# Kernel optimization log

Hardware: AMD Instinct MI355X
Metric: run time of the kernel (lower is better)

The kernel has to match this reference:

```python
import jax, jax.numpy as jnp
import numpy as np

TGT, BSZ, E = 2048, 4, 1024
NUM_HEADS = 16
HEAD_DIM = E // NUM_HEADS


def setup_inputs() -> dict:
    key = jax.random.key(0)
    ks = jax.random.split(key, 5)
    return {
        "query": jax.random.normal(ks[0], (TGT, BSZ, E), dtype=jnp.float32),
        "key": jax.random.normal(ks[1], (TGT, BSZ, E), dtype=jnp.float32),
        "value": jax.random.normal(ks[2], (TGT, BSZ, E), dtype=jnp.float32),
        "in_proj_weight": jax.random.normal(ks[3], (3 * E, E), dtype=jnp.float32) * (1.0 / np.sqrt(E)),
        "in_proj_bias": jnp.zeros((3 * E,), dtype=jnp.float32),
        "out_proj_weight": jax.random.normal(ks[4], (E, E), dtype=jnp.float32) * (1.0 / np.sqrt(E)),
        "out_proj_bias": jnp.zeros((E,), dtype=jnp.float32),
    }


def reference(query, key, value, in_proj_weight, in_proj_bias, out_proj_weight, out_proj_bias):
    tgt_len, bsz, embed_dim = query.shape
    src_len = key.shape[0]
    h, hd = NUM_HEADS, embed_dim // NUM_HEADS

    w_q, w_k, w_v = jnp.split(in_proj_weight, 3, axis=0)
    b_q, b_k, b_v = jnp.split(in_proj_bias, 3, axis=0)
    q = query @ w_q.T + b_q   # (Nt, B, E)
    k = key @ w_k.T + b_k     # (Ns, B, E)
    v = value @ w_v.T + b_v

    # (L, B, E) -> (B*H, L, hd)
    q = q.reshape(tgt_len, bsz * h, hd).transpose(1, 0, 2)
    k = k.reshape(src_len, bsz * h, hd).transpose(1, 0, 2)
    v = v.reshape(src_len, bsz * h, hd).transpose(1, 0, 2)

    q = q / jnp.sqrt(jnp.asarray(hd, dtype=q.dtype))
    attn = jnp.einsum('bte,bse->bts', q, k)          # (B*H, Nt, Ns)
    attn = jax.nn.softmax(attn, axis=-1)
    out = jnp.einsum('bts,bse->bte', attn, v)        # (B*H, Nt, hd)

    out = out.transpose(1, 0, 2).reshape(tgt_len, bsz, embed_dim)
    out = out @ out_proj_weight.T + out_proj_bias    # (Nt, B, out_dim)

    avg_weights = attn.reshape(bsz, h, tgt_len, src_len).mean(axis=1)
    return (out, avg_weights)
```

## Files before the change

kernel.cpp:

```cpp
#include <hip/hip_runtime.h>
#include <hip/hip_bf16.h>
#include <hip/hip_fp16.h>

#define TGT 2048
#define BSZ 4
#define EMB 1024
#define NH  16
#define HD  64
#define NTOK (TGT*BSZ)
#define BH   (BSZ*NH)

typedef unsigned short u16;
typedef __attribute__((ext_vector_type(8)))  short        s16x8;
typedef __attribute__((ext_vector_type(8)))  _Float16     f16x8;
typedef __attribute__((ext_vector_type(2)))  _Float16     f16x2;
typedef __attribute__((ext_vector_type(2)))  __fp16       fp16x2;
typedef __attribute__((ext_vector_type(4)))  float        f32x4;
typedef __attribute__((ext_vector_type(16))) float        f32x16;
typedef __attribute__((ext_vector_type(4)))  unsigned int u32x4;

#define MFMA_BF16(a,b,c)  __builtin_amdgcn_mfma_f32_16x16x32_bf16(a,b,c,0,0,0)
#define MFMA_F16(a,b,c)   __builtin_amdgcn_mfma_f32_16x16x32_f16(a,b,c,0,0,0)
#define MFMA32_F16(a,b,c) __builtin_amdgcn_mfma_f32_32x32x16_f16(a,b,c,0,0,0)

#define GLOAD_LDS16(gsrc, ldst) \
  __builtin_amdgcn_global_load_lds((const __attribute__((address_space(1))) unsigned int*)(gsrc), \
                                   (__attribute__((address_space(3))) unsigned int*)(ldst), 16, 0, 0)

__device__ __forceinline__ void split_one(float x, u16& h, u16& l) {
  __hip_bfloat16 hb = __float2bfloat16(x);
  float hf = __bfloat162float(hb);
  __hip_bfloat16 lb = __float2bfloat16(x - hf);
  h = *reinterpret_cast<u16*>(&hb);
  l = *reinterpret_cast<u16*>(&lb);
}

__global__ __launch_bounds__(256) void split_kernel(const float* __restrict__ x,
    u16* __restrict__ hi, u16* __restrict__ lo, int n4) {
  int i = blockIdx.x * 256 + threadIdx.x;
  if (i >= n4) return;
  float4 v = reinterpret_cast<const float4*>(x)[i];
  ushort4 h, l;
  split_one(v.x, h.x, l.x);
  split_one(v.y, h.y, l.y);
  split_one(v.z, h.z, l.z);
  split_one(v.w, h.w, l.w);
  reinterpret_cast<ushort4*>(hi)[i] = h;
  reinterpret_cast<ushort4*>(lo)[i] = l;
}

template<int EPI>
__global__ __launch_bounds__(256) void gemm_split(
    const u16* __restrict__ Ah, const u16* __restrict__ Al,
    const u16* __restrict__ Bh, const u16* __restrict__ Bl,
    const float* __restrict__ bias, float scale, void* __restrict__ outp, int K)
{
  __shared__ __align__(16) u16 As[128*64];
  __shared__ __align__(16) u16 Bs[128*64];
  const int tid  = threadIdx.x;
  const int bm0  = blockIdx.y * 128;
  const int bn0  = blockIdx.x * 128;
  const int wave = tid >> 6, lane = tid & 63, lr = lane & 15, lg = lane >> 4;

  f32x4 zero = {0.f, 0.f, 0.f, 0.f};
  f32x4 acc[2][8];
  #pragma unroll
  for (int i = 0; i < 2; i++)
    #pragma unroll
    for (int j = 0; j < 8; j++) acc[i][j] = zero;

  const u16* srcA[4];
  const u16* srcB[4];
  #pragma unroll
  for (int j = 0; j < 4; j++) {
    int gi  = tid + j*256;
    int row = gi >> 3;
    int lgc = (gi & 7) ^ (row & 7);
    const u16* baA = (lgc < 4) ? Ah : Al;
    const u16* baB = (lgc < 4) ? Bh : Bl;
    srcA[j] = baA + (size_t)(bm0 + row)*K + (lgc & 3)*8;
    srcB[j] = baB + (size_t)(bn0 + row)*K + (lgc & 3)*8;
  }
  char* AsB = (char*)As;
  char* BsB = (char*)Bs;
  const int ldsb = wave*1024;

  for (int kt = 0; kt < K; kt += 32) {
    __syncthreads();
    #pragma unroll
    for (int j = 0; j < 4; j++) {
      GLOAD_LDS16(srcA[j] + kt, AsB + ldsb + j*4096);
      GLOAD_LDS16(srcB[j] + kt, BsB + ldsb + j*4096);
    }
    __syncthreads();

    s16x8 ah[2], al2[2];
    #pragma unroll
    for (int mf = 0; mf < 2; mf++) {
      int row = wave*32 + mf*16 + lr;
      const char* rb = AsB + row*128;
      ah[mf]  = *(const s16x8*)(rb + (((lg    ) ^ (row & 7)) << 4));
      al2[mf] = *(const s16x8*)(rb + (((lg | 4) ^ (row & 7)) << 4));
    }
    #pragma unroll
    for (int nf = 0; nf < 8; nf++) {
      int row = nf*16 + lr;
      const char* rb = BsB + row*128;
      s16x8 bh8 = *(const s16x8*)(rb + (((lg    ) ^ (row & 7)) << 4));
      s16x8 bl8 = *(const s16x8*)(rb + (((lg | 4) ^ (row & 7)) << 4));
      #pragma unroll
      for (int mf = 0; mf < 2; mf++) {
        acc[mf][nf] = MFMA_BF16(al2[mf], bh8, acc[mf][nf]);
        acc[mf][nf] = MFMA_BF16(ah[mf],  bl8, acc[mf][nf]);
        acc[mf][nf] = MFMA_BF16(ah[mf],  bh8, acc[mf][nf]);
      }
    }
  }
  #pragma unroll
  for (int mf = 0; mf < 2; mf++)
    #pragma unroll
    for (int nf = 0; nf < 8; nf++)
      #pragma unroll
      for (int r = 0; r < 4; r++) {
        int m = bm0 + wave*32 + mf*16 + lg*4 + r;
        int n = bn0 + nf*16 + lr;
        float v = (acc[mf][nf][r] + bias[n]) * scale;
        if constexpr (EPI == 0) {
          int t = m >> 2, b = m & 3, h = n >> 6, d = n & 63;
          ((_Float16*)outp)[(size_t)((b*NH + h)*TGT + t)*HD + d] = (_Float16)v;
        } else if constexpr (EPI == 1) {
          int s = m >> 2, b = m & 3, h = n >> 6, d = n & 63;
          ((_Float16*)outp)[(size_t)((b*NH + h)*HD + d)*TGT + s] = (_Float16)v;
        } else {
          ((float*)outp)[(size_t)m*EMB + n] = v;
        }
      }
}

__global__ __launch_bounds__(256) void flash_kernel(
    const _Float16* __restrict__ Qf, const _Float16* __restrict__ Kf,
    const _Float16* __restrict__ Vt, u16* __restrict__ Oh, u16* __restrict__ Ol,
    float* __restrict__ lse)
{
  __shared__ __align__(16) _Float16 Ks[64*64];
  __shared__ __align__(16) _Float16 Vs[64*64];
  const int tid = threadIdx.x, wq = tid >> 6, lane = tid & 63;
  const int lt = lane & 31, hl = lane >> 5;
  const int bh = blockIdx.y, t0 = blockIdx.x * 128;
  const int b = bh >> 4, h = bh & 15;
  const int t = t0 + wq*32 + lt;

  f16x8 qf[4];
  #pragma unroll
  for (int kk = 0; kk < 4; kk++)
    qf[kk] = *(const f16x8*)&Qf[((size_t)bh*TGT + t)*HD + kk*16 + hl*8];

  float m_run = -1e30f, l_run = 0.f;
  f32x16 accO[2];
  #pragma unroll
  for (int i = 0; i < 16; i++) { accO[0][i] = 0.f; accO[1][i] = 0.f; }

  char* KsB = (char*)Ks;
  char* VsB = (char*)Vs;

  for (int s0 = 0; s0 < TGT; s0 += 64) {
    __syncthreads();
    #pragma unroll
    for (int j = 0; j < 2; j++) {
      int gi = tid + j*256;
      int row = gi >> 3, sg = (gi & 7) ^ (row & 7);
      GLOAD_LDS16(Kf + ((size_t)bh*TGT + s0 + row)*HD + sg*8, KsB + wq*1024 + j*4096);
      GLOAD_LDS16(Vt + ((size_t)bh*HD + row)*TGT + s0 + sg*8, VsB + wq*1024 + j*4096);
    }
    __syncthreads();

    f32x16 sacc[2];
    #pragma unroll
    for (int i = 0; i < 16; i++) { sacc[0][i] = 0.f; sacc[1][i] = 0.f; }
    #pragma unroll
    for (int sf = 0; sf < 2; sf++)
      #pragma unroll
      for (int kk = 0; kk < 4; kk++) {
        int row = sf*32 + lt;
        int g = (2*kk + hl) ^ (row & 7);
        f16x8 kfr = *(const f16x8*)(KsB + row*128 + g*16);
        sacc[sf] = MFMA32_F16(kfr, qf[kk], sacc[sf]);
      }

    float pm = -1e30f;
    #pragma unroll
    for (int sf = 0; sf < 2; sf++)
      #pragma unroll
      for (int r = 0; r < 16; r++) pm = fmaxf(pm, sacc[sf][r]);
    pm = fmaxf(pm, __shfl_xor(pm, 32, 64));
    float m_new = fmaxf(m_run, pm);
    float fsc = exp2f(m_run - m_new);
    float psum = 0.f;
    #pragma unroll
    for (int sf = 0; sf < 2; sf++)
      #pragma unroll
      for (int r = 0; r < 16; r++) {
        float p = exp2f(sacc[sf][r] - m_new);
        sacc[sf][r] = p;
        psum += p;
      }
    psum += __shfl_xor(psum, 32, 64);
    l_run = l_run * fsc + psum;
    m_run = m_new;
    accO[0] *= fsc;
    accO[1] *= fsc;

    #pragma unroll
    for (int sf = 0; sf < 2; sf++) {
      unsigned int P0[4], P1[4];
      #pragma unroll
      for (int q = 0; q < 4; q++) {
        union { fp16x2 h2; unsigned int u; } c0, c1;
        c0.h2 = __builtin_amdgcn_cvt_pkrtz(sacc[sf][4*q],     sacc[sf][4*q + 1]);
        c1.h2 = __builtin_amdgcn_cvt_pkrtz(sacc[sf][4*q + 2], sacc[sf][4*q + 3]);
        P0[q] = c0.u;
        P1[q] = c1.u;
      }
      #pragma unroll
      for (int mp = 0; mp < 2; mp++) {
        unsigned int a0 = P0[2*mp], b0 = P0[2*mp + 1];
        unsigned int a1 = P1[2*mp], b1 = P1[2*mp + 1];
        asm("v_permlane32_swap_b32 %0, %1" : "+v"(a0), "+v"(b0));
        asm("v_permlane32_swap_b32 %0, %1" : "+v"(a1), "+v"(b1));
        union { u32x4 u; f16x8 f; } pw;
        pw.u = (u32x4){a0, a1, b0, b1};
        const int m = sf*2 + mp;
        #pragma unroll
        for (int df = 0; df < 2; df++) {
          int row = df*32 + lt;
          int g = (2*m + hl) ^ (row & 7);
          f16x8 vfr = *(const f16x8*)(VsB + row*128 + g*16);
          accO[df] = MFMA32_F16(vfr, pw.f, accO[df]);
        }
      }
    }
  }

  float linv = 1.f / l_run;
  #pragma unroll
  for (int df = 0; df < 2; df++)
    #pragma unroll
    for (int q = 0; q < 4; q++) {
      ushort4 hs, ls;
      float o0 = accO[df][4*q]     * linv;
      float o1 = accO[df][4*q + 1] * linv;
      float o2 = accO[df][4*q + 2] * linv;
      float o3 = accO[df][4*q + 3] * linv;
      split_one(o0, hs.x, ls.x);
      split_one(o1, hs.y, ls.y);
      split_one(o2, hs.z, ls.z);
      split_one(o3, hs.w, ls.w);
      int d0 = 32*df + 8*q + 4*hl;
      size_t idx = ((size_t)t*BSZ + b)*EMB + h*HD + d0;
      *(ushort4*)&Oh[idx] = hs;
      *(ushort4*)&Ol[idx] = ls;
    }
  if (hl == 0)
    lse[(size_t)bh*TGT + t] = m_run + log2f(l_run);
}

__global__ __launch_bounds__(256) void avg_kernel(
    const _Float16* __restrict__ Qf, const _Float16* __restrict__ Kf,
    const float* __restrict__ lse, float* __restrict__ avgO)
{
  __shared__ __align__(16) _Float16 Qs[128][64];
  __shared__ __align__(16) _Float16 Ks[128][64];
  __shared__ float lses[NH][128];
  const int tid = threadIdx.x, wave = tid >> 6, lane = tid & 63, lr = lane & 15, lg = lane >> 4;

  int fid = blockIdx.x;
  int nid = (fid & 7) * 128 + (fid >> 3);
  int st = nid & 15, tt = (nid >> 4) & 15, b = nid >> 8;
  int s0 = st * 128, t0 = tt * 128;

  #pragma unroll
  for (int i = 0; i < 8; i++) {
    int idx = tid + i * 256;
    int hh = idx >> 7, t = idx & 127;
    lses[hh][t] = lse[(size_t)(b*NH + hh)*TGT + t0 + t];
  }

  f32x4 zero = {0.f, 0.f, 0.f, 0.f};
  f32x4 acc[2][8];
  #pragma unroll
  for (int i = 0; i < 2; i++)
    #pragma unroll
    for (int j = 0; j < 8; j++) acc[i][j] = zero;

  const int rQ = wave * 32;
  const int srcsub = (((lane & 7) ^ (lane >> 3)) << 4) + (lane >> 3) * 128;

  for (int h = 0; h < NH; h++) {
    __syncthreads();
    {
      const char* qb = (const char*)(Qf + ((size_t)(b*NH + h)*TGT + t0) * HD);
      const char* kb = (const char*)(Kf + ((size_t)(b*NH + h)*TGT + s0) * HD);
      const char* gb = (wave < 2) ? qb : kb;
      char* lb = (char*)((wave < 2) ? &Qs[0][0] : &Ks[0][0]);
      const int half = (wave & 1) * 8;
      #pragma unroll
      for (int j = 0; j < 8; j++) {
        int J = half + j;
        GLOAD_LDS16(gb + (size_t)J * 1024 + srcsub, lb + J * 1024);
      }
    }
    __syncthreads();

    float lsr[2][4];
    #pragma unroll
    for (int mf = 0; mf < 2; mf++)
      #pragma unroll
      for (int r = 0; r < 4; r++)
        lsr[mf][r] = lses[h][rQ + mf*16 + lg*4 + r];

    f16x8 aq[2][2];
    #pragma unroll
    for (int mf = 0; mf < 2; mf++)
      #pragma unroll
      for (int kf = 0; kf < 2; kf++) {
        int row = rQ + mf*16 + lr;
        int cb = ((kf*4 + lg) ^ (row & 7)) << 4;
        aq[mf][kf] = *(const f16x8*)((const char*)&Qs[0][0] + row*128 + cb);
      }
    #pragma unroll
    for (int nf = 0; nf < 8; nf++) {
      f32x4 s4[2] = {zero, zero};
      #pragma unroll
      for (int kf = 0; kf < 2; kf++) {
        int row = nf*16 + lr;
        int cb = ((kf*4 + lg) ^ (row & 7)) << 4;
        f16x8 bk = *(const f16x8*)((const char*)&Ks[0][0] + row*128 + cb);
        s4[0] = MFMA_F16(aq[0][kf], bk, s4[0]);
        s4[1] = MFMA_F16(aq[1][kf], bk, s4[1]);
      }
      #pragma unroll
      for (int mf = 0; mf < 2; mf++)
        #pragma unroll
        for (int r = 0; r < 4; r++)
          acc[mf][nf][r] += exp2f(s4[mf][r] - lsr[mf][r]);
    }
  }

  #pragma unroll
  for (int mf = 0; mf < 2; mf++)
    #pragma unroll
    for (int nf = 0; nf < 8; nf++)
      #pragma unroll
      for (int r = 0; r < 4; r++) {
        int ti = t0 + rQ + mf*16 + lg*4 + r;
        int sj = s0 + nf*16 + lr;
        avgO[((size_t)b*TGT + ti)*TGT + sj] = acc[mf][nf][r] * (1.f/16.f);
      }
}

extern "C" void kernel_launch(void* const* d_in, const int* in_sizes, int n_in,
                              void* d_out, int out_size, void* d_ws, size_t ws_size,
                              hipStream_t stream) {
  const float* query = (const float*)d_in[0];
  const float* key_  = (const float*)d_in[1];
  const float* value = (const float*)d_in[2];
  const float* ipw   = (const float*)d_in[3];
  const float* ipb   = (const float*)d_in[4];
  const float* opw   = (const float*)d_in[5];
  const float* opb   = (const float*)d_in[6];
  float* out = (float*)d_out;
  float* avg = out + (size_t)TGT*BSZ*EMB;

  char* ws = (char*)d_ws;
  size_t o = 0;
  auto alloc = [&](size_t bytes) { char* p = ws + o; o += bytes; return p; };
  u16* Wh  = (u16*)alloc((size_t)3*EMB*EMB*2);
  u16* Wl  = (u16*)alloc((size_t)3*EMB*EMB*2);
  u16* Woh = (u16*)alloc((size_t)EMB*EMB*2);
  u16* Wol = (u16*)alloc((size_t)EMB*EMB*2);
  u16* Xh  = (u16*)alloc((size_t)NTOK*EMB*2);
  u16* Xl  = (u16*)alloc((size_t)NTOK*EMB*2);
  _Float16* Qf = (_Float16*)alloc((size_t)NTOK*EMB*2);
  _Float16* Kf = (_Float16*)alloc((size_t)NTOK*EMB*2);
  _Float16* Vt = (_Float16*)alloc((size_t)NTOK*EMB*2);
  u16* OhA = (u16*)alloc((size_t)NTOK*EMB*2);
  u16* OlA = (u16*)alloc((size_t)NTOK*EMB*2);
  float* lseA = (float*)alloc((size_t)BH*TGT*4);
  (void)ws_size; (void)in_sizes; (void)n_in; (void)out_size;

  const float QSCALE = 0.18033688011112042f;

  split_kernel<<<3*EMB*EMB/1024, 256, 0, stream>>>(ipw, Wh, Wl, 3*EMB*EMB/4);
  split_kernel<<<EMB*EMB/1024, 256, 0, stream>>>(opw, Woh, Wol, EMB*EMB/4);

  dim3 ggrid(EMB/128, NTOK/128);
  split_kernel<<<NTOK*EMB/1024, 256, 0, stream>>>(query, Xh, Xl, NTOK*EMB/4);
  gemm_split<0><<<ggrid, 256, 0, stream>>>(Xh, Xl, Wh, Wl, ipb, QSCALE, (void*)Qf, EMB);
  split_kernel<<<NTOK*EMB/1024, 256, 0, stream>>>(key_, Xh, Xl, NTOK*EMB/4);
  gemm_split<0><<<ggrid, 256, 0, stream>>>(Xh, Xl, Wh + (size_t)EMB*EMB, Wl + (size_t)EMB*EMB,
                                           ipb + EMB, 1.0f, (void*)Kf, EMB);
  split_kernel<<<NTOK*EMB/1024, 256, 0, stream>>>(value, Xh, Xl, NTOK*EMB/4);
  gemm_split<1><<<ggrid, 256, 0, stream>>>(Xh, Xl, Wh + (size_t)2*EMB*EMB, Wl + (size_t)2*EMB*EMB,
                                           ipb + 2*EMB, 1.0f, (void*)Vt, EMB);

  flash_kernel<<<dim3(TGT/128, BH), 256, 0, stream>>>(Qf, Kf, Vt, OhA, OlA, lseA);
  avg_kernel<<<1024, 256, 0, stream>>>(Qf, Kf, lseA, avg);
  gemm_split<2><<<ggrid, 256, 0, stream>>>(OhA, OlA, Woh, Wol, opb, 1.0f, (void*)out, EMB);
}
```

Baseline: 666.3 us.

## Double-buffer LDS tiles in split GEMM and flash attention kernels

Both the split-bf16 GEMM and the flash attention kernel now keep two LDS buffers and issue the global-to-LDS loads for the next K/V or K-tile before computing on the current one. Partial vmcnt waits and raw s_barrier replace the paired __syncthreads, so memory latency can overlap with MFMA work. This doubles shared memory per block (64KB for the GEMM), which can cut occupancy, and it relies on the hand-set vmcnt counts matching the number of outstanding loads.

```diff
diff --git a/kernel.cpp b/kernel.cpp
--- a/kernel.cpp
+++ b/kernel.cpp
@@ -55,8 +55,8 @@
     const u16* __restrict__ Bh, const u16* __restrict__ Bl,
     const float* __restrict__ bias, float scale, void* __restrict__ outp, int K)
 {
-  __shared__ __align__(16) u16 As[128*64];
-  __shared__ __align__(16) u16 Bs[128*64];
+  __shared__ __align__(16) u16 As[2][128*64];
+  __shared__ __align__(16) u16 Bs[2][128*64];
   const int tid  = threadIdx.x;
   const int bm0  = blockIdx.y * 128;
   const int bn0  = blockIdx.x * 128;
@@ -81,19 +81,38 @@
     srcA[j] = baA + (size_t)(bm0 + row)*K + (lgc & 3)*8;
     srcB[j] = baB + (size_t)(bn0 + row)*K + (lgc & 3)*8;
   }
-  char* AsB = (char*)As;
-  char* BsB = (char*)Bs;
   const int ldsb = wave*1024;
-
-  for (int kt = 0; kt < K; kt += 32) {
-    __syncthreads();
+  const int NT = K >> 5;
+
+  {
+    char* AsB = (char*)As[0];
+    char* BsB = (char*)Bs[0];
     #pragma unroll
     for (int j = 0; j < 4; j++) {
-      GLOAD_LDS16(srcA[j] + kt, AsB + ldsb + j*4096);
-      GLOAD_LDS16(srcB[j] + kt, BsB + ldsb + j*4096);
-    }
-    __syncthreads();
-
+      GLOAD_LDS16(srcA[j], AsB + ldsb + j*4096);
+      GLOAD_LDS16(srcB[j], BsB + ldsb + j*4096);
+    }
+  }
+
+  for (int t = 0; t < NT; ++t) {
+    const int cur = t & 1;
+    if (t + 1 < NT) {
+      char* AsB = (char*)As[cur ^ 1];
+      char* BsB = (char*)Bs[cur ^ 1];
+      const int kt = (t + 1) << 5;
+      #pragma unroll
+      for (int j = 0; j < 4; j++) {
+        GLOAD_LDS16(srcA[j] + kt, AsB + ldsb + j*4096);
+        GLOAD_LDS16(srcB[j] + kt, BsB + ldsb + j*4096);
+      }
+      asm volatile("s_waitcnt vmcnt(8)" ::: "memory");
+    } else {
+      asm volatile("s_waitcnt vmcnt(0)" ::: "memory");
+    }
+    __builtin_amdgcn_s_barrier();
+
+    const char* AsB = (const char*)As[cur];
+    const char* BsB = (const char*)Bs[cur];
     s16x8 ah[2], al2[2];
     #pragma unroll
     for (int mf = 0; mf < 2; mf++) {
@@ -115,7 +134,11 @@
         acc[mf][nf] = MFMA_BF16(ah[mf],  bh8, acc[mf][nf]);
       }
     }
-  }
+    asm volatile("s_waitcnt lgkmcnt(0)" ::: "memory");
+    __builtin_amdgcn_sched_barrier(0);
+    __builtin_amdgcn_s_barrier();
+  }
+
   #pragma unroll
   for (int mf = 0; mf < 2; mf++)
     #pragma unroll
@@ -142,8 +165,8 @@
     const _Float16* __restrict__ Vt, u16* __restrict__ Oh, u16* __restrict__ Ol,
     float* __restrict__ lse)
 {
-  __shared__ __align__(16) _Float16 Ks[64*64];
-  __shared__ __align__(16) _Float16 Vs[64*64];
+  __shared__ __align__(16) _Float16 Ks[2][64*64];
+  __shared__ __align__(16) _Float16 Vs[2][64*64];
   const int tid = threadIdx.x, wq = tid >> 6, lane = tid & 63;
   const int lt = lane & 31, hl = lane >> 5;
   const int bh = blockIdx.y, t0 = blockIdx.x * 128;
@@ -160,19 +183,42 @@
   #pragma unroll
   for (int i = 0; i < 16; i++) { accO[0][i] = 0.f; accO[1][i] = 0.f; }
 
-  char* KsB = (char*)Ks;
-  char* VsB = (char*)Vs;
-
-  for (int s0 = 0; s0 < TGT; s0 += 64) {
-    __syncthreads();
-    #pragma unroll
-    for (int j = 0; j < 2; j++) {
-      int gi = tid + j*256;
-      int row = gi >> 3, sg = (gi & 7) ^ (row & 7);
-      GLOAD_LDS16(Kf + ((size_t)bh*TGT + s0 + row)*HD + sg*8, KsB + wq*1024 + j*4096);
-      GLOAD_LDS16(Vt + ((size_t)bh*HD + row)*TGT + s0 + sg*8, VsB + wq*1024 + j*4096);
-    }
-    __syncthreads();
+  const int gi0 = tid,       row0 = gi0 >> 3, sg0 = (gi0 & 7) ^ (row0 & 7);
+  const int gi1 = tid + 256, row1 = gi1 >> 3, sg1 = (gi1 & 7) ^ (row1 & 7);
+  const _Float16* kp0 = Kf + ((size_t)bh*TGT + row0)*HD + sg0*8;
+  const _Float16* kp1 = Kf + ((size_t)bh*TGT + row1)*HD + sg1*8;
+  const _Float16* vp0 = Vt + ((size_t)bh*HD + row0)*TGT + sg0*8;
+  const _Float16* vp1 = Vt + ((size_t)bh*HD + row1)*TGT + sg1*8;
+
+  {
+    char* kb = (char*)Ks[0] + wq*1024;
+    char* vb = (char*)Vs[0] + wq*1024;
+    GLOAD_LDS16(kp0, kb);
+    GLOAD_LDS16(kp1, kb + 4096);
+    GLOAD_LDS16(vp0, vb);
+    GLOAD_LDS16(vp1, vb + 4096);
+  }
+
+  const int NKV = TGT / 64;
+  for (int it = 0; it < NKV; ++it) {
+    const int cur = it & 1;
+    if (it + 1 < NKV) {
+      const size_t ko = (size_t)(it + 1) * 64 * HD;
+      const size_t vo = (size_t)(it + 1) * 64;
+      char* kb = (char*)Ks[cur ^ 1] + wq*1024;
+      char* vb = (char*)Vs[cur ^ 1] + wq*1024;
+      GLOAD_LDS16(kp0 + ko, kb);
+      GLOAD_LDS16(kp1 + ko, kb + 4096);
+      GLOAD_LDS16(vp0 + vo, vb);
+      GLOAD_LDS16(vp1 + vo, vb + 4096);
+      asm volatile("s_waitcnt vmcnt(4)" ::: "memory");
+    } else {
+      asm volatile("s_waitcnt vmcnt(0)" ::: "memory");
+    }
+    __builtin_amdgcn_s_barrier();
+
+    const char* KsB = (const char*)Ks[cur];
+    const char* VsB = (const char*)Vs[cur];
 
     f32x16 sacc[2];
     #pragma unroll
@@ -239,6 +285,10 @@
         }
       }
     }
+
+    asm volatile("s_waitcnt lgkmcnt(0)" ::: "memory");
+    __builtin_amdgcn_sched_barrier(0);
+    __builtin_amdgcn_s_barrier();
   }
 
   float linv = 1.f / l_run;
```

After: 681.9 us. 1.02x slower.
